# Optimization experiments

Hardware: AMD Instinct MI355X
Metric: run time of the kernel (lower is better)

Reference implementation:

```python
import jax, jax.numpy as jnp
import numpy as np

BRIGHT_THRESH = 0.65
SAT_THRESH = 0.15
SMOOTH_K = 15
LAMBDA_L1 = 1.0
LAMBDA_WIN_L1 = 3.0
LAMBDA_WIN_COLOR = 1.0
WINDOW_WEIGHT = 5.0
BASE_WEIGHT = 1.0
TRANSFORM_WEIGHT = 2.0
EPS = 1e-8


def _avg_pool_same(x, k=SMOOTH_K):
    # AvgPool2d(k, stride=1, padding=k//2), count_include_pad=True (torch default)
    p = k // 2
    s = jax.lax.reduce_window(x, 0.0, jax.lax.add, (1, 1, k, k), (1, 1, 1, 1),
                              [(0, 0), (0, 0), (p, p), (p, p)])
    return s / (k * k)


def _window_detector(source):
    # Rescale from [-1,1] to [0,1] if any negative values present
    src = jnp.where(source.min() < 0, (source + 1) * 0.5, source)
    brightness = 0.299 * src[:, 0:1] + 0.587 * src[:, 1:2] + 0.114 * src[:, 2:3]
    bright_mask = jax.nn.sigmoid(20.0 * (brightness - BRIGHT_THRESH))
    saturation = src.max(axis=1, keepdims=True) - src.min(axis=1, keepdims=True)
    low_sat_mask = jax.nn.sigmoid(20.0 * (SAT_THRESH - saturation))
    return _avg_pool_same(bright_mask * low_sat_mask)


def _normalize_ch(x):
    # F.normalize over channel dim with eps clamp
    n = jnp.sqrt(jnp.sum(x * x, axis=1, keepdims=True))
    return x / jnp.maximum(n, EPS)


def setup_inputs() -> dict:
    key = jax.random.key(0)
    k1, k2, k3 = jax.random.split(key, 3)
    shape = (16, 3, 512, 512)
    return {
        "pred": jax.random.normal(k1, shape, dtype=jnp.float32),
        "target": jax.random.normal(k2, shape, dtype=jnp.float32),
        "source": jax.random.normal(k3, shape, dtype=jnp.float32),
    }


def reference(pred, target, source):
    window_mask = _window_detector(source)  # [B,1,H,W]

    # plain L1
    l1_loss = jnp.abs(pred - target).mean()

    # window-weighted L1
    weight_map = BASE_WEIGHT + (WINDOW_WEIGHT - BASE_WEIGHT) * window_mask
    win_l1_loss = (jnp.abs(pred - target) * weight_map).mean()

    # window color-transform loss
    st = target - source  # source -> target direction
    sp = pred - source    # source -> pred direction
    alignment = jnp.sum(_normalize_ch(st) * _normalize_ch(sp), axis=1, keepdims=True)
    st_mag = jnp.sqrt(jnp.sum(st * st, axis=1, keepdims=True))
    sp_mag = jnp.sqrt(jnp.sum(sp * sp, axis=1, keepdims=True))
    mag_loss = jnp.abs(sp_mag / (st_mag + EPS) - 1.0)
    color_loss = TRANSFORM_WEIGHT * (window_mask * (1.0 - alignment + 0.5 * mag_loss)).mean()

    total = LAMBDA_L1 * l1_loss + LAMBDA_WIN_L1 * win_l1_loss + LAMBDA_WIN_COLOR * color_loss
    return total
```

## Files before the change

### kernel.cpp

```cpp
#include <hip/hip_runtime.h>
#include <math.h>

#define W 512
#define H 512
#define BATCH 16
#define HW (W * H)
#define NPIX (BATCH * HW)
#define NELEM (3 * NPIX)

#define TW 64
#define TH 32
#define TILES_X (W / TW)
#define TILES_Y (H / TH)
#define TILES_PER_IMG (TILES_X * TILES_Y)
#define NBLOCKS (BATCH * TILES_PER_IMG)

#define MROWS (TH + 14)
#define MCOLS (TW + 14)
#define MSTRIDE 81
#define HSTRIDE 68

__global__ __launch_bounds__(256, 4) void k_fused(const float* __restrict__ pred,
                                                  const float* __restrict__ targ,
                                                  const float* __restrict__ srcp,
                                                  float* __restrict__ partials) {
    __shared__ float smask[MROWS * MSTRIDE];
    __shared__ __align__(16) float shsum[MROWS * HSTRIDE];

    const int tid = threadIdx.x;
    const int bid = blockIdx.x;
    const int b  = bid >> 7;
    const int tl = bid & 127;
    const int ty = tl >> 3;
    const int tx = tl & 7;
    const int y0 = ty * TH;
    const int x0 = tx * TW;
    const size_t ibase = (size_t)b * 3 * HW;

    for (int idx = tid; idx < MROWS * MCOLS; idx += 256) {
        const int row = idx / MCOLS;
        const int col = idx - row * MCOLS;
        const int gy = y0 - 7 + row;
        const int gx = x0 - 7 + col;
        float mval = 0.f;
        if ((unsigned)gy < (unsigned)H && (unsigned)gx < (unsigned)W) {
            const size_t o = ibase + (size_t)gy * W + gx;
            const float R = (srcp[o]          + 1.f) * 0.5f;
            const float G = (srcp[o + HW]     + 1.f) * 0.5f;
            const float B = (srcp[o + 2 * HW] + 1.f) * 0.5f;
            const float bright = 0.299f * R + 0.587f * G + 0.114f * B;
            const float sat = fmaxf(R, fmaxf(G, B)) - fminf(R, fminf(G, B));
            const float bm = 1.f / (1.f + __expf(-20.f * (bright - 0.65f)));
            const float sm = 1.f / (1.f + __expf(-20.f * (0.15f - sat)));
            mval = bm * sm;
        }
        smask[row * MSTRIDE + col] = mval;
    }
    __syncthreads();

    if (tid < MROWS * 2) {
        const int r = tid >> 1;
        const int h = tid & 1;
        const float* mr = smask + r * MSTRIDE + 32 * h;
        float* hr = shsum + r * HSTRIDE + 32 * h;
        float acc = 0.f;
#pragma unroll
        for (int k = 0; k < 15; ++k) acc += mr[k];
        for (int i = 0; i < 32; ++i) {
            hr[i] = acc;
            if (i < 31) acc += mr[i + 15] - mr[i];
        }
    }
    __syncthreads();

    const int cg = tid & 15;
    const int rg = tid >> 4;
    const int ro0 = 2 * rg;
    const int gx = x0 + 4 * cg;

    float4 S = make_float4(0.f, 0.f, 0.f, 0.f);
#pragma unroll
    for (int k = 0; k < 15; ++k) {
        const float4 hv = *(const float4*)(shsum + (ro0 + k) * HSTRIDE + 4 * cg);
        S.x += hv.x; S.y += hv.y; S.z += hv.z; S.w += hv.w;
    }

    float sA = 0.f, sAW = 0.f, sC = 0.f;
    const float inv225 = 1.f / 225.f;

#pragma unroll
    for (int i = 0; i < 2; ++i) {
        const int ro = ro0 + i;
        if (i == 1) {
            const float4 hadd = *(const float4*)(shsum + (ro0 + 15) * HSTRIDE + 4 * cg);
            const float4 hsub = *(const float4*)(shsum + ro0 * HSTRIDE + 4 * cg);
            S.x += hadd.x - hsub.x; S.y += hadd.y - hsub.y;
            S.z += hadd.z - hsub.z; S.w += hadd.w - hsub.w;
        }
        const float wm[4] = {S.x * inv225, S.y * inv225, S.z * inv225, S.w * inv225};

        const size_t base = ibase + (size_t)(y0 + ro) * W + gx;
        const float4 pR = *(const float4*)(pred + base);
        const float4 pG = *(const float4*)(pred + base + HW);
        const float4 pB = *(const float4*)(pred + base + 2 * HW);
        const float4 tR = *(const float4*)(targ + base);
        const float4 tG = *(const float4*)(targ + base + HW);
        const float4 tB = *(const float4*)(targ + base + 2 * HW);
        const float4 sR = *(const float4*)(srcp + base);
        const float4 sG = *(const float4*)(srcp + base + HW);
        const float4 sB = *(const float4*)(srcp + base + 2 * HW);

        const float pr[4] = {pR.x, pR.y, pR.z, pR.w}, pg[4] = {pG.x, pG.y, pG.z, pG.w},
                    pb[4] = {pB.x, pB.y, pB.z, pB.w};
        const float tr[4] = {tR.x, tR.y, tR.z, tR.w}, tg[4] = {tG.x, tG.y, tG.z, tG.w},
                    tb[4] = {tB.x, tB.y, tB.z, tB.w};
        const float sr[4] = {sR.x, sR.y, sR.z, sR.w}, sg[4] = {sG.x, sG.y, sG.z, sG.w},
                    sb[4] = {sB.x, sB.y, sB.z, sB.w};

#pragma unroll
        for (int j = 0; j < 4; ++j) {
            const float a = fabsf(pr[j] - tr[j]) + fabsf(pg[j] - tg[j]) + fabsf(pb[j] - tb[j]);
            const float stx = tr[j] - sr[j], sty = tg[j] - sg[j], stz = tb[j] - sb[j];
            const float spx = pr[j] - sr[j], spy = pg[j] - sg[j], spz = pb[j] - sb[j];
            const float dot = stx * spx + sty * spy + stz * spz;
            const float stm = sqrtf(stx * stx + sty * sty + stz * stz);
            const float spm = sqrtf(spx * spx + spy * spy + spz * spz);
            const float align = dot / (fmaxf(stm, 1e-8f) * fmaxf(spm, 1e-8f));
            const float mag = fabsf(spm / (stm + 1e-8f) - 1.f);
            const float c = 1.f - align + 0.5f * mag;
            sA  += a;
            sAW += a * wm[j];
            sC  += c * wm[j];
        }
    }

#pragma unroll
    for (int off = 32; off > 0; off >>= 1) {
        sA  += __shfl_down(sA, off);
        sAW += __shfl_down(sAW, off);
        sC  += __shfl_down(sC, off);
    }
    __shared__ float red[3][4];
    const int lane = tid & 63;
    const int wave = tid >> 6;
    if (lane == 0) { red[0][wave] = sA; red[1][wave] = sAW; red[2][wave] = sC; }
    __syncthreads();
    if (tid == 0) {
        partials[(size_t)bid * 3 + 0] = red[0][0] + red[0][1] + red[0][2] + red[0][3];
        partials[(size_t)bid * 3 + 1] = red[1][0] + red[1][1] + red[1][2] + red[1][3];
        partials[(size_t)bid * 3 + 2] = red[2][0] + red[2][1] + red[2][2] + red[2][3];
    }
}

__global__ __launch_bounds__(256) void k_final(const float* __restrict__ partials,
                                               float* __restrict__ out) {
    double a = 0.0, aw = 0.0, c = 0.0;
    for (int i = threadIdx.x; i < NBLOCKS; i += 256) {
        a  += (double)partials[(size_t)i * 3 + 0];
        aw += (double)partials[(size_t)i * 3 + 1];
        c  += (double)partials[(size_t)i * 3 + 2];
    }
#pragma unroll
    for (int off = 32; off > 0; off >>= 1) {
        a  += __shfl_down(a, off);
        aw += __shfl_down(aw, off);
        c  += __shfl_down(c, off);
    }
    __shared__ double rd[3][4];
    const int lane = threadIdx.x & 63;
    const int wave = threadIdx.x >> 6;
    if (lane == 0) { rd[0][wave] = a; rd[1][wave] = aw; rd[2][wave] = c; }
    __syncthreads();
    if (threadIdx.x == 0) {
        const double A  = rd[0][0] + rd[0][1] + rd[0][2] + rd[0][3];
        const double AW = rd[1][0] + rd[1][1] + rd[1][2] + rd[1][3];
        const double C  = rd[2][0] + rd[2][1] + rd[2][2] + rd[2][3];
        const double N = (double)NELEM;
        const double M = (double)NPIX;
        out[0] = (float)((4.0 * A + 12.0 * AW) / N + 2.0 * C / M);
    }
}

extern "C" void kernel_launch(void* const* d_in, const int* in_sizes, int n_in,
                              void* d_out, int out_size, void* d_ws, size_t ws_size,
                              hipStream_t stream) {
    const float* pred = (const float*)d_in[0];
    const float* targ = (const float*)d_in[1];
    const float* src  = (const float*)d_in[2];

    float* partials = (float*)d_ws;

    k_fused<<<NBLOCKS, 256, 0, stream>>>(pred, targ, src, partials);
    k_final<<<1, 256, 0, stream>>>(partials, (float*)d_out);
}
```

Measured before the change: 173.8 us.

## Vectorize mask halo loads, parallelize horizontal box sum, hoist loads, use fast math

The mask halo is now loaded as float4 vectors over an 80-wide window, replacing scalar per-pixel loads. The sequential per-row horizontal sliding sum, which used only 92 threads, is replaced by a direct 15-tap sum with one thread per output column. All 18 pred/target/source float4 loads for both rows are issued before the vertical shared-memory sum so their latency overlaps it. Division and sqrt are swapped for hardware rcp/sqrt intrinsics, which lowers precision slightly and raises register pressure.

```diff
diff --git a/kernel.cpp b/kernel.cpp
--- a/kernel.cpp
+++ b/kernel.cpp
@@ -10,112 +10,138 @@
 
 #define TW 64
 #define TH 32
-#define TILES_X (W / TW)
-#define TILES_Y (H / TH)
-#define TILES_PER_IMG (TILES_X * TILES_Y)
-#define NBLOCKS (BATCH * TILES_PER_IMG)
-
-#define MROWS (TH + 14)
-#define MCOLS (TW + 14)
-#define MSTRIDE 81
+#define NBLOCKS 2048
+
+#define MROWS 46
+#define MCOLS 80
+#define HCOLS 64
 #define HSTRIDE 68
+
+__device__ __forceinline__ float fast_rcp(float x)  { return __builtin_amdgcn_rcpf(x); }
+__device__ __forceinline__ float fast_sqrt(float x) { return __builtin_amdgcn_sqrtf(x); }
+
+__device__ __forceinline__ float maskval(float r, float g, float b) {
+    const float R = (r + 1.f) * 0.5f;
+    const float G = (g + 1.f) * 0.5f;
+    const float B = (b + 1.f) * 0.5f;
+    const float bright = 0.299f * R + 0.587f * G + 0.114f * B;
+    const float sat = fmaxf(R, fmaxf(G, B)) - fminf(R, fminf(G, B));
+    const float bm = fast_rcp(1.f + __expf(-20.f * (bright - 0.65f)));
+    const float sm = fast_rcp(1.f + __expf(-20.f * (0.15f - sat)));
+    return bm * sm;
+}
 
 __global__ __launch_bounds__(256, 4) void k_fused(const float* __restrict__ pred,
                                                   const float* __restrict__ targ,
                                                   const float* __restrict__ srcp,
                                                   float* __restrict__ partials) {
-    __shared__ float smask[MROWS * MSTRIDE];
+    __shared__ __align__(16) float smask[MROWS * MCOLS];
     __shared__ __align__(16) float shsum[MROWS * HSTRIDE];
 
     const int tid = threadIdx.x;
     const int bid = blockIdx.x;
     const int b  = bid >> 7;
     const int tl = bid & 127;
-    const int ty = tl >> 3;
-    const int tx = tl & 7;
-    const int y0 = ty * TH;
-    const int x0 = tx * TW;
+    const int y0 = (tl >> 3) * TH;
+    const int x0 = (tl & 7) * TW;
     const size_t ibase = (size_t)b * 3 * HW;
 
-    for (int idx = tid; idx < MROWS * MCOLS; idx += 256) {
-        const int row = idx / MCOLS;
-        const int col = idx - row * MCOLS;
-        const int gy = y0 - 7 + row;
-        const int gx = x0 - 7 + col;
-        float mval = 0.f;
-        if ((unsigned)gy < (unsigned)H && (unsigned)gx < (unsigned)W) {
-            const size_t o = ibase + (size_t)gy * W + gx;
-            const float R = (srcp[o]          + 1.f) * 0.5f;
-            const float G = (srcp[o + HW]     + 1.f) * 0.5f;
-            const float B = (srcp[o + 2 * HW] + 1.f) * 0.5f;
-            const float bright = 0.299f * R + 0.587f * G + 0.114f * B;
-            const float sat = fmaxf(R, fmaxf(G, B)) - fminf(R, fminf(G, B));
-            const float bm = 1.f / (1.f + __expf(-20.f * (bright - 0.65f)));
-            const float sm = 1.f / (1.f + __expf(-20.f * (0.15f - sat)));
-            mval = bm * sm;
+#pragma unroll
+    for (int p0 = 0; p0 < 1024; p0 += 256) {
+        const int p = p0 + tid;
+        if (p < MROWS * 20) {
+            const int r = p / 20;
+            const int q = p - r * 20;
+            const int gy = y0 - 7 + r;
+            const int gx = x0 - 8 + 4 * q;
+            float4 mv = make_float4(0.f, 0.f, 0.f, 0.f);
+            if ((unsigned)gy < (unsigned)H && (unsigned)gx < (unsigned)W) {
+                const size_t o = ibase + (size_t)gy * W + gx;
+                const float4 R4 = *(const float4*)(srcp + o);
+                const float4 G4 = *(const float4*)(srcp + o + HW);
+                const float4 B4 = *(const float4*)(srcp + o + 2 * HW);
+                mv.x = maskval(R4.x, G4.x, B4.x);
+                mv.y = maskval(R4.y, G4.y, B4.y);
+                mv.z = maskval(R4.z, G4.z, B4.z);
+                mv.w = maskval(R4.w, G4.w, B4.w);
+            }
+            *(float4*)(smask + r * MCOLS + 4 * q) = mv;
         }
-        smask[row * MSTRIDE + col] = mval;
-    }
-    __syncthreads();
-
-    if (tid < MROWS * 2) {
-        const int r = tid >> 1;
-        const int h = tid & 1;
-        const float* mr = smask + r * MSTRIDE + 32 * h;
-        float* hr = shsum + r * HSTRIDE + 32 * h;
-        float acc = 0.f;
-#pragma unroll
-        for (int k = 0; k < 15; ++k) acc += mr[k];
-        for (int i = 0; i < 32; ++i) {
-            hr[i] = acc;
-            if (i < 31) acc += mr[i + 15] - mr[i];
+    }
+    __syncthreads();
+
+#pragma unroll
+    for (int p0 = 0; p0 < MROWS * HCOLS; p0 += 256) {
+        const int p = p0 + tid;
+        if (p < MROWS * HCOLS) {
+            const int r = p >> 6;
+            const int c = p & 63;
+            const float* mr = smask + r * MCOLS + c + 1;
+            float s = 0.f;
+#pragma unroll
+            for (int k = 0; k < 15; ++k) s += mr[k];
+            shsum[r * HSTRIDE + c] = s;
         }
     }
     __syncthreads();
 
     const int cg = tid & 15;
     const int rg = tid >> 4;
-    const int ro0 = 2 * rg;
-    const int gx = x0 + 4 * cg;
-
-    float4 S = make_float4(0.f, 0.f, 0.f, 0.f);
+    const int ro = 2 * rg;
+    const size_t base0 = ibase + (size_t)(y0 + ro) * W + (x0 + 4 * cg);
+    const size_t base1 = base0 + W;
+
+    const float4 pA0 = *(const float4*)(pred + base0);
+    const float4 pB0 = *(const float4*)(pred + base0 + HW);
+    const float4 pC0 = *(const float4*)(pred + base0 + 2 * HW);
+    const float4 tA0 = *(const float4*)(targ + base0);
+    const float4 tB0 = *(const float4*)(targ + base0 + HW);
+    const float4 tC0 = *(const float4*)(targ + base0 + 2 * HW);
+    const float4 sA0 = *(const float4*)(srcp + base0);
+    const float4 sB0 = *(const float4*)(srcp + base0 + HW);
+    const float4 sC0 = *(const float4*)(srcp + base0 + 2 * HW);
+    const float4 pA1 = *(const float4*)(pred + base1);
+    const float4 pB1 = *(const float4*)(pred + base1 + HW);
+    const float4 pC1 = *(const float4*)(pred + base1 + 2 * HW);
+    const float4 tA1 = *(const float4*)(targ + base1);
+    const float4 tB1 = *(const float4*)(targ + base1 + HW);
+    const float4 tC1 = *(const float4*)(targ + base1 + 2 * HW);
+    const float4 sA1 = *(const float4*)(srcp + base1);
+    const float4 sB1 = *(const float4*)(srcp + base1 + HW);
+    const float4 sC1 = *(const float4*)(srcp + base1 + 2 * HW);
+
+    const float* hcol = shsum + 4 * cg;
+    float4 S0 = make_float4(0.f, 0.f, 0.f, 0.f);
 #pragma unroll
     for (int k = 0; k < 15; ++k) {
-        const float4 hv = *(const float4*)(shsum + (ro0 + k) * HSTRIDE + 4 * cg);
-        S.x += hv.x; S.y += hv.y; S.z += hv.z; S.w += hv.w;
-    }
-
+        const float4 h = *(const float4*)(hcol + (ro + k) * HSTRIDE);
+        S0.x += h.x; S0.y += h.y; S0.z += h.z; S0.w += h.w;
+    }
+    const float4 hsub = *(const float4*)(hcol + ro * HSTRIDE);
+    const float4 hadd = *(const float4*)(hcol + (ro + 15) * HSTRIDE);
+    const float4 S1 = make_float4(S0.x - hsub.x + hadd.x, S0.y - hsub.y + hadd.y,
+                                  S0.z - hsub.z + hadd.z, S0.w - hsub.w + hadd.w);
+
+    const float inv225 = 1.f / 225.f;
     float sA = 0.f, sAW = 0.f, sC = 0.f;
-    const float inv225 = 1.f / 225.f;
 
 #pragma unroll
     for (int i = 0; i < 2; ++i) {
-        const int ro = ro0 + i;
-        if (i == 1) {
-            const float4 hadd = *(const float4*)(shsum + (ro0 + 15) * HSTRIDE + 4 * cg);
-            const float4 hsub = *(const float4*)(shsum + ro0 * HSTRIDE + 4 * cg);
-            S.x += hadd.x - hsub.x; S.y += hadd.y - hsub.y;
-            S.z += hadd.z - hsub.z; S.w += hadd.w - hsub.w;
-        }
-        const float wm[4] = {S.x * inv225, S.y * inv225, S.z * inv225, S.w * inv225};
-
-        const size_t base = ibase + (size_t)(y0 + ro) * W + gx;
-        const float4 pR = *(const float4*)(pred + base);
-        const float4 pG = *(const float4*)(pred + base + HW);
-        const float4 pB = *(const float4*)(pred + base + 2 * HW);
-        const float4 tR = *(const float4*)(targ + base);
-        const float4 tG = *(const float4*)(targ + base + HW);
-        const float4 tB = *(const float4*)(targ + base + 2 * HW);
-        const float4 sR = *(const float4*)(srcp + base);
-        const float4 sG = *(const float4*)(srcp + base + HW);
-        const float4 sB = *(const float4*)(srcp + base + 2 * HW);
-
-        const float pr[4] = {pR.x, pR.y, pR.z, pR.w}, pg[4] = {pG.x, pG.y, pG.z, pG.w},
-                    pb[4] = {pB.x, pB.y, pB.z, pB.w};
-        const float tr[4] = {tR.x, tR.y, tR.z, tR.w}, tg[4] = {tG.x, tG.y, tG.z, tG.w},
-                    tb[4] = {tB.x, tB.y, tB.z, tB.w};
-        const float sr[4] = {sR.x, sR.y, sR.z, sR.w}, sg[4] = {sG.x, sG.y, sG.z, sG.w},
-                    sb[4] = {sB.x, sB.y, sB.z, sB.w};
+        const float4 Pv[3] = {i ? pA1 : pA0, i ? pB1 : pB0, i ? pC1 : pC0};
+        const float4 Tv[3] = {i ? tA1 : tA0, i ? tB1 : tB0, i ? tC1 : tC0};
+        const float4 Sv[3] = {i ? sA1 : sA0, i ? sB1 : sB0, i ? sC1 : sC0};
+        const float4 Sw = i ? S1 : S0;
+        const float wm[4] = {Sw.x * inv225, Sw.y * inv225, Sw.z * inv225, Sw.w * inv225};
+
+        const float pr[4] = {Pv[0].x, Pv[0].y, Pv[0].z, Pv[0].w};
+        const float pg[4] = {Pv[1].x, Pv[1].y, Pv[1].z, Pv[1].w};
+        const float pb[4] = {Pv[2].x, Pv[2].y, Pv[2].z, Pv[2].w};
+        const float tr[4] = {Tv[0].x, Tv[0].y, Tv[0].z, Tv[0].w};
+        const float tg[4] = {Tv[1].x, Tv[1].y, Tv[1].z, Tv[1].w};
+        const float tb[4] = {Tv[2].x, Tv[2].y, Tv[2].z, Tv[2].w};
+        const float sr[4] = {Sv[0].x, Sv[0].y, Sv[0].z, Sv[0].w};
+        const float sg[4] = {Sv[1].x, Sv[1].y, Sv[1].z, Sv[1].w};
+        const float sb[4] = {Sv[2].x, Sv[2].y, Sv[2].z, Sv[2].w};
 
 #pragma unroll
         for (int j = 0; j < 4; ++j) {
@@ -123,10 +149,10 @@
             const float stx = tr[j] - sr[j], sty = tg[j] - sg[j], stz = tb[j] - sb[j];
             const float spx = pr[j] - sr[j], spy = pg[j] - sg[j], spz = pb[j] - sb[j];
             const float dot = stx * spx + sty * spy + stz * spz;
-            const float stm = sqrtf(stx * stx + sty * sty + stz * stz);
-            const float spm = sqrtf(spx * spx + spy * spy + spz * spz);
-            const float align = dot / (fmaxf(stm, 1e-8f) * fmaxf(spm, 1e-8f));
-            const float mag = fabsf(spm / (stm + 1e-8f) - 1.f);
+            const float stm = fast_sqrt(stx * stx + sty * sty + stz * stz);
+            const float spm = fast_sqrt(spx * spx + spy * spy + spz * spz);
+            const float align = dot * fast_rcp(fmaxf(stm, 1e-8f) * fmaxf(spm, 1e-8f));
+            const float mag = fabsf(spm * fast_rcp(stm + 1e-8f) - 1.f);
             const float c = 1.f - align + 0.5f * mag;
             sA  += a;
             sAW += a * wm[j];
```

Result: faster. 168.6 us (-3.0%).
